# Kernel tuning notes

Measured on AMD Instinct MI355X. Metric: run time of the kernel, lower is better.

The kernel has to match this reference:

```python
import jax, jax.numpy as jnp
import numpy as np


def _apply_ring(x, angles):
    """Apply x @ R^T where R = G_0 @ G_1 @ ... @ G_{n-1} with ring planes
    (k, (k+1) % n). Equivalent to applying G_k^T to x for k = n-1 .. 0:
      x[:, k] <- c*x[:, k] - s*x[:, j]
      x[:, j] <- s*x[:, k] + c*x[:, j]
    x: [B, n], angles: [n].
    """
    n = angles.shape[0]

    def step(xT, k):
        a = angles[k]
        c, s = jnp.cos(a), jnp.sin(a)
        j = jnp.mod(k + 1, n)
        xi = xT[k]
        xj = xT[j]
        xT = xT.at[k].set(c * xi - s * xj)
        xT = xT.at[j].set(s * xi + c * xj)
        return xT, None

    ks = jnp.arange(n - 1, -1, -1)  # reverse order: R^T = G_{n-1}^T ... G_0^T
    xT, _ = jax.lax.scan(step, x.T, ks)  # carry is [n, B]
    return xT.T


def setup_inputs() -> dict:
    key = jax.random.key(0)
    k_x, k_e, k_d = jax.random.split(key, 3)
    B, n, num_blocks = 8192, 1024, 4
    return {
        "x": jax.random.normal(k_x, (B, n), dtype=jnp.float32),
        "angles_enc": jax.random.normal(k_e, (num_blocks, n), dtype=jnp.float32),
        "angles_dec": jax.random.normal(k_d, (num_blocks, n), dtype=jnp.float32),
        "hidden_weight": jnp.zeros((1,), dtype=jnp.float32),
        "hidden_state": jnp.zeros((n,), dtype=jnp.float32),
    }


def reference(x, angles_enc, angles_dec, hidden_weight, hidden_state):
    num_blocks = angles_enc.shape[0]
    b = x
    for blk in range(num_blocks):
        b = _apply_ring(b, angles_enc[blk])
    # recurrent blend; weight uses the detached hidden_weight (original uses
    # numpy on .detach()), so stop_gradient matches the original semantics.
    w = jax.nn.sigmoid(jax.lax.stop_gradient(hidden_weight[0]))
    bottleneck = (1.0 - w) * b + w * hidden_state[None, :]
    out = bottleneck
    for blk in range(num_blocks):
        out = _apply_ring(out, angles_dec[blk])
    return (bottleneck, out)
```

## Files before the change

### kernel.cpp

```cpp
#include <hip/hip_runtime.h>
#include <math.h>

#define N_COLS 1024
#define TPR    16
#define CHUNK  64
#define ROWS_PER_BLOCK 16
#define NRINGS 8

__global__ __launch_bounds__(256, 2)
void ClassicalEncoderDecoder_57080115363917_kernel(
        const float* __restrict__ x,
        const float* __restrict__ ae,
        const float* __restrict__ ad,
        const float* __restrict__ hw,
        const float* __restrict__ hs,
        float* __restrict__ out, int B)
{
    __shared__ float2 s_cs[NRINGS * CHUNK * TPR];
    __shared__ float  s_A [NRINGS * TPR];
    __shared__ float2 s_aux[NRINGS];

    const int tid = threadIdx.x;

    for (int i = 0; i < 32; ++i) {
        int idx = i * 256 + tid;
        int r   = idx >> 10;
        int k   = idx & 1023;
        const float* ang = (r < 4) ? (ae + (r << 10)) : (ad + ((r - 4) << 10));
        float a = ang[k];
        float sv, cv;
        sincosf(a, &sv, &cv);
        int t = k >> 6, j = k & 63;
        float2 e = make_float2(cv, sv);
        if (k == 1023) {
            s_aux[r] = e;
            e = make_float2(0.f, -1.f);
        }
        s_cs[(r * CHUNK + j) * TPR + t] = e;
    }
    __syncthreads();
    if (tid < NRINGS * TPR) {
        int r = tid >> 4, t = tid & 15;
        float p = 1.f;
        for (int j = 0; j < CHUNK; ++j) p *= -s_cs[(r * CHUNK + j) * TPR + t].y;
        s_A[tid] = p;
    }
    __syncthreads();

    const int lane      = tid & 63;
    const int g         = lane >> 4;
    const int t         = lane & 15;
    const int groupBase = lane & 48;
    const int row       = blockIdx.x * ROWS_PER_BLOCK + (tid >> 6) * 4 + g;

    const float* xr = x + (size_t)row * N_COLS + t * CHUNK;
    float y[CHUNK];
    #pragma unroll
    for (int i = 0; i < 16; ++i) {
        float4 v = ((const float4*)xr)[i];
        y[4*i+0] = v.x; y[4*i+1] = v.y; y[4*i+2] = v.z; y[4*i+3] = v.w;
    }

    const float w   = 1.f / (1.f + expf(-hw[0]));
    const float omw = 1.f - w;

    for (int r = 0; r < NRINGS; ++r) {
        if (r == 4) {
            float4* ob = (float4*)(out + (size_t)row * N_COLS + t * CHUNK);
            const float4* hp = (const float4*)(hs + t * CHUNK);
            #pragma unroll
            for (int i = 0; i < 16; ++i) {
                float4 h = hp[i];
                float4 bn;
                bn.x = fmaf(omw, y[4*i+0], w * h.x);
                bn.y = fmaf(omw, y[4*i+1], w * h.y);
                bn.z = fmaf(omw, y[4*i+2], w * h.z);
                bn.w = fmaf(omw, y[4*i+3], w * h.w);
                ob[i] = bn;
                y[4*i+0] = bn.x; y[4*i+1] = bn.y; y[4*i+2] = bn.z; y[4*i+3] = bn.w;
            }
        }

        const float2* csr = s_cs + r * CHUNK * TPR;
        const float2  cN  = s_aux[r];

        float y0 = __shfl(y[0],  groupBase);
        float yN = __shfl(y[63], groupBase + 15);
        float Cinit = cN.x * yN - cN.y * y0;
        float x0n   = fmaf(cN.y, yN, cN.x * y0);
        if (t == 0) y[0] = x0n;

        float carry = 0.f;
        float ztmp  = 0.f;
        #pragma unroll
        for (int j = CHUNK - 1; j >= 0; --j) {
            float2 cs = csr[j * TPR + t];
            float z   = fmaf(cs.y, y[j], cs.x * carry);
            carry     = fmaf(-cs.y, carry, cs.x * y[j]);
            if (j == CHUNK - 1) ztmp = z; else y[j + 1] = z;
        }

        float sa = s_A[r * TPR + t], sb = carry;
        #pragma unroll
        for (int d = 1; d < 16; d <<= 1) {
            float a2 = __shfl_down(sa, d);
            float b2 = __shfl_down(sb, d);
            if (t + d < 16) { sb = fmaf(sa, b2, sb); sa *= a2; }
        }
        float ea = __shfl_down(sa, 1);
        float eb = __shfl_down(sb, 1);
        float z0  = fmaf(sa, Cinit, sb);
        float Cin = (t == 15) ? Cinit : fmaf(ea, Cinit, eb);

        float P = 1.f;
        #pragma unroll
        for (int j = CHUNK - 1; j >= 0; --j) {
            float2 cs = csr[j * TPR + t];
            float f = cs.x * P;
            P = -cs.y * P;
            if (j == CHUNK - 1) ztmp = fmaf(f, Cin, ztmp);
            else                y[j + 1] = fmaf(f, Cin, y[j + 1]);
        }

        float up = __shfl_up(ztmp, 1);
        y[0] = (t == 0) ? z0 : up;
    }

    float4* oo = (float4*)(out + (size_t)B * N_COLS + (size_t)row * N_COLS + t * CHUNK);
    #pragma unroll
    for (int i = 0; i < 16; ++i) {
        float4 v;
        v.x = y[4*i+0]; v.y = y[4*i+1]; v.z = y[4*i+2]; v.w = y[4*i+3];
        oo[i] = v;
    }
}

extern "C" void kernel_launch(void* const* d_in, const int* in_sizes, int n_in,
                              void* d_out, int out_size, void* d_ws, size_t ws_size,
                              hipStream_t stream) {
    const float* x  = (const float*)d_in[0];
    const float* ae = (const float*)d_in[1];
    const float* ad = (const float*)d_in[2];
    const float* hw = (const float*)d_in[3];
    const float* hs = (const float*)d_in[4];
    float* out = (float*)d_out;

    const int B = in_sizes[0] / N_COLS;
    dim3 grid(B / ROWS_PER_BLOCK), block(256);
    hipLaunchKernelGGL(ClassicalEncoderDecoder_57080115363917_kernel,
                       grid, block, 0, stream, x, ae, ad, hw, hs, out, B);
}
```

Before: 133.3 us.

## Precompute Givens coefficients in a setup kernel and halve per-thread chunk size

Adds a small setup kernel that computes sin/cos, the propagation factors and the chunk products once into workspace, so the main kernel no longer repeats the sincos work and shared-memory staging in every block. The main kernel uses 32 threads per row with 32-element chunks, which cuts per-thread register pressure enough to raise launch bounds to 4 blocks per SM. Coefficients are read as float4 from global/L2 instead of LDS, and the scan now has 5 shuffle steps instead of 4. The old kernel is kept as a fallback when the workspace is too small.

```diff
diff --git a/kernel.cpp b/kernel.cpp
--- a/kernel.cpp
+++ b/kernel.cpp
@@ -2,47 +2,200 @@
 #include <math.h>
 
 #define N_COLS 1024
-#define TPR    16
-#define CHUNK  64
-#define ROWS_PER_BLOCK 16
 #define NRINGS 8
 
+#define TPR    32
+#define CHUNK  32
+#define ROWS_PER_BLOCK 8
+
+#define F_OFF   16384
+#define A_OFF   24576
+#define AUX_OFF 24832
+#define WS_FLOATS 24848
+
+__global__ void ced_setup(const float* __restrict__ ae,
+                          const float* __restrict__ ad,
+                          float* __restrict__ ws)
+{
+    __shared__ float2 ls[N_COLS];
+    const int r   = blockIdx.x;
+    const int tid = threadIdx.x;
+    const float* ang = (r < 4) ? (ae + (r << 10)) : (ad + ((r - 4) << 10));
+
+    #pragma unroll
+    for (int m = 0; m < 4; ++m) {
+        int k = tid * 4 + m;
+        float sv, cv;
+        sincosf(ang[k], &sv, &cv);
+        if (k == N_COLS - 1) {
+            ((float2*)(ws + AUX_OFF))[r] = make_float2(cv, sv);
+            cv = 0.f; sv = -1.f;
+        }
+        ls[k] = make_float2(cv, sv);
+    }
+    __syncthreads();
+
+    {
+        int k0 = tid * 4;
+        int t  = k0 >> 5;
+        int jp = (k0 & 31) >> 1;
+        float4* CS = (float4*)ws;
+        float2 e0 = ls[k0], e1 = ls[k0+1], e2 = ls[k0+2], e3 = ls[k0+3];
+        CS[(r*16 + jp    )*32 + t] = make_float4(e0.x, e0.y, e1.x, e1.y);
+        CS[(r*16 + jp + 1)*32 + t] = make_float4(e2.x, e2.y, e3.x, e3.y);
+    }
+
+    if (tid < TPR) {
+        int t = tid;
+        float f[CHUNK];
+        float P = 1.f;
+        for (int j = CHUNK - 1; j >= 0; --j) {
+            float2 cs = ls[t*CHUNK + j];
+            f[j] = cs.x * P;
+            P    = -cs.y * P;
+        }
+        float4* F = (float4*)(ws + F_OFF);
+        #pragma unroll
+        for (int qi = 0; qi < 8; ++qi)
+            F[(r*8 + qi)*32 + t] = make_float4(f[4*qi], f[4*qi+1], f[4*qi+2], f[4*qi+3]);
+        ws[A_OFF + r*TPR + t] = P;
+    }
+}
+
+__global__ __launch_bounds__(256, 4)
+void ced_main(const float* __restrict__ x,
+              const float* __restrict__ ws,
+              const float* __restrict__ hw,
+              const float* __restrict__ hs,
+              float* __restrict__ out, int B)
+{
+    const float4* CS  = (const float4*)ws;
+    const float4* F   = (const float4*)(ws + F_OFF);
+    const float*  A   = ws + A_OFF;
+    const float2* AUX = (const float2*)(ws + AUX_OFF);
+
+    const int tid  = threadIdx.x;
+    const int lane = tid & 63;
+    const int t    = lane & 31;
+    const int g    = lane >> 5;
+    const int groupBase = lane & 32;
+    const int row  = blockIdx.x * ROWS_PER_BLOCK + (tid >> 6) * 2 + g;
+
+    float y[CHUNK];
+    const float4* xp = (const float4*)(x + (size_t)row * N_COLS + t * CHUNK);
+    #pragma unroll
+    for (int i = 0; i < 8; ++i) {
+        float4 v = xp[i];
+        y[4*i] = v.x; y[4*i+1] = v.y; y[4*i+2] = v.z; y[4*i+3] = v.w;
+    }
+
+    const float w   = 1.f / (1.f + expf(-hw[0]));
+    const float omw = 1.f - w;
+
+    #pragma unroll 1
+    for (int r = 0; r < NRINGS; ++r) {
+        if (r == 4) {
+            float4* ob = (float4*)(out + (size_t)row * N_COLS + t * CHUNK);
+            const float4* hp = (const float4*)(hs + t * CHUNK);
+            #pragma unroll
+            for (int i = 0; i < 8; ++i) {
+                float4 h = hp[i];
+                float4 bn;
+                bn.x = fmaf(omw, y[4*i+0], w * h.x);
+                bn.y = fmaf(omw, y[4*i+1], w * h.y);
+                bn.z = fmaf(omw, y[4*i+2], w * h.z);
+                bn.w = fmaf(omw, y[4*i+3], w * h.w);
+                ob[i] = bn;
+                y[4*i+0] = bn.x; y[4*i+1] = bn.y; y[4*i+2] = bn.z; y[4*i+3] = bn.w;
+            }
+        }
+
+        const float2 cN = AUX[r];
+        float y0 = __shfl(y[0],       groupBase);
+        float yN = __shfl(y[CHUNK-1], groupBase + 31);
+        float Cinit = cN.x * yN - cN.y * y0;
+        float x0n   = fmaf(cN.y, yN, cN.x * y0);
+        if (t == 0) y[0] = x0n;
+
+        float carry = 0.f, ztmp = 0.f;
+        const float4* csr = CS + r * 512 + t;
+        #pragma unroll
+        for (int jp = CHUNK/2 - 1; jp >= 0; --jp) {
+            float4 cs4 = csr[jp * 32];
+            const int j1 = 2*jp + 1;
+            float z1 = fmaf(cs4.w, y[j1], cs4.z * carry);
+            carry    = fmaf(-cs4.w, carry, cs4.z * y[j1]);
+            if (j1 == CHUNK - 1) ztmp = z1; else y[j1+1] = z1;
+            const int j0 = 2*jp;
+            float z0s = fmaf(cs4.y, y[j0], cs4.x * carry);
+            carry     = fmaf(-cs4.y, carry, cs4.x * y[j0]);
+            y[j0+1] = z0s;
+        }
+
+        float sa = A[r*32 + t];
+        float sb = carry;
+        #pragma unroll
+        for (int d = 1; d < TPR; d <<= 1) {
+            float a2 = __shfl_down(sa, d);
+            float b2 = __shfl_down(sb, d);
+            if (t + d < TPR) { sb = fmaf(sa, b2, sb); sa *= a2; }
+        }
+        float ea = __shfl_down(sa, 1), eb = __shfl_down(sb, 1);
+        float zfirst = fmaf(sa, Cinit, sb);
+        float Cin = (t == TPR - 1) ? Cinit : fmaf(ea, Cinit, eb);
+
+        const float4* fr = F + r * 256 + t;
+        #pragma unroll
+        for (int qi = CHUNK/4 - 1; qi >= 0; --qi) {
+            float4 f4 = fr[qi * 32];
+            const int j = 4*qi;
+            if (j + 3 == CHUNK - 1) ztmp   = fmaf(f4.w, Cin, ztmp);
+            else                    y[j+4] = fmaf(f4.w, Cin, y[j+4]);
+            y[j+3] = fmaf(f4.z, Cin, y[j+3]);
+            y[j+2] = fmaf(f4.y, Cin, y[j+2]);
+            y[j+1] = fmaf(f4.x, Cin, y[j+1]);
+        }
+
+        float up = __shfl_up(ztmp, 1);
+        y[0] = (t == 0) ? zfirst : up;
+    }
+
+    float4* oo = (float4*)(out + (size_t)B * N_COLS + (size_t)row * N_COLS + t * CHUNK);
+    #pragma unroll
+    for (int i = 0; i < 8; ++i)
+        oo[i] = make_float4(y[4*i], y[4*i+1], y[4*i+2], y[4*i+3]);
+}
+
 __global__ __launch_bounds__(256, 2)
-void ClassicalEncoderDecoder_57080115363917_kernel(
-        const float* __restrict__ x,
-        const float* __restrict__ ae,
-        const float* __restrict__ ad,
-        const float* __restrict__ hw,
-        const float* __restrict__ hs,
-        float* __restrict__ out, int B)
+void ced_fallback(const float* __restrict__ x,
+                  const float* __restrict__ ae,
+                  const float* __restrict__ ad,
+                  const float* __restrict__ hw,
+                  const float* __restrict__ hs,
+                  float* __restrict__ out, int B)
 {
-    __shared__ float2 s_cs[NRINGS * CHUNK * TPR];
-    __shared__ float  s_A [NRINGS * TPR];
+    __shared__ float2 s_cs[NRINGS * 64 * 16];
+    __shared__ float  s_A [NRINGS * 16];
     __shared__ float2 s_aux[NRINGS];
 
     const int tid = threadIdx.x;
-
     for (int i = 0; i < 32; ++i) {
         int idx = i * 256 + tid;
         int r   = idx >> 10;
         int k   = idx & 1023;
         const float* ang = (r < 4) ? (ae + (r << 10)) : (ad + ((r - 4) << 10));
-        float a = ang[k];
         float sv, cv;
-        sincosf(a, &sv, &cv);
+        sincosf(ang[k], &sv, &cv);
         int t = k >> 6, j = k & 63;
         float2 e = make_float2(cv, sv);
-        if (k == 1023) {
-            s_aux[r] = e;
-            e = make_float2(0.f, -1.f);
-        }
-        s_cs[(r * CHUNK + j) * TPR + t] = e;
+        if (k == 1023) { s_aux[r] = e; e = make_float2(0.f, -1.f); }
+        s_cs[(r * 64 + j) * 16 + t] = e;
     }
     __syncthreads();
-    if (tid < NRINGS * TPR) {
+    if (tid < NRINGS * 16) {
         int r = tid >> 4, t = tid & 15;
         float p = 1.f;
-        for (int j = 0; j < CHUNK; ++j) p *= -s_cs[(r * CHUNK + j) * TPR + t].y;
+        for (int j = 0; j < 64; ++j) p *= -s_cs[(r * 64 + j) * 16 + t].y;
         s_A[tid] = p;
     }
     __syncthreads();
@@ -51,23 +204,22 @@
     const int g         = lane >> 4;
     const int t         = lane & 15;
     const int groupBase = lane & 48;
-    const int row       = blockIdx.x * ROWS_PER_BLOCK + (tid >> 6) * 4 + g;
-
-    const float* xr = x + (size_t)row * N_COLS + t * CHUNK;
-    float y[CHUNK];
+    const int row       = blockIdx.x * 16 + (tid >> 6) * 4 + g;
+
+    const float* xr = x + (size_t)row * N_COLS + t * 64;
+    float y[64];
     #pragma unroll
     for (int i = 0; i < 16; ++i) {
         float4 v = ((const float4*)xr)[i];
-        y[4*i+0] = v.x; y[4*i+1] = v.y; y[4*i+2] = v.z; y[4*i+3] = v.w;
-    }
-
+        y[4*i] = v.x; y[4*i+1] = v.y; y[4*i+2] = v.z; y[4*i+3] = v.w;
+    }
     const float w   = 1.f / (1.f + expf(-hw[0]));
     const float omw = 1.f - w;
 
     for (int r = 0; r < NRINGS; ++r) {
         if (r == 4) {
-            float4* ob = (float4*)(out + (size_t)row * N_COLS + t * CHUNK);
-            const float4* hp = (const float4*)(hs + t * CHUNK);
+            float4* ob = (float4*)(out + (size_t)row * N_COLS + t * 64);
+            const float4* hp = (const float4*)(hs + t * 64);
             #pragma unroll
             for (int i = 0; i < 16; ++i) {
                 float4 h = hp[i];
@@ -80,27 +232,23 @@
                 y[4*i+0] = bn.x; y[4*i+1] = bn.y; y[4*i+2] = bn.z; y[4*i+3] = bn.w;
             }
         }
-
-        const float2* csr = s_cs + r * CHUNK * TPR;
+        const float2* csr = s_cs + r * 64 * 16;
         const float2  cN  = s_aux[r];
-
         float y0 = __shfl(y[0],  groupBase);
         float yN = __shfl(y[63], groupBase + 15);
         float Cinit = cN.x * yN - cN.y * y0;
         float x0n   = fmaf(cN.y, yN, cN.x * y0);
         if (t == 0) y[0] = x0n;
 
-        float carry = 0.f;
-        float ztmp  = 0.f;
-        #pragma unroll
-        for (int j = CHUNK - 1; j >= 0; --j) {
-            float2 cs = csr[j * TPR + t];
+        float carry = 0.f, ztmp = 0.f;
+        #pragma unroll
+        for (int j = 63; j >= 0; --j) {
+            float2 cs = csr[j * 16 + t];
             float z   = fmaf(cs.y, y[j], cs.x * carry);
             carry     = fmaf(-cs.y, carry, cs.x * y[j]);
-            if (j == CHUNK - 1) ztmp = z; else y[j + 1] = z;
-        }
-
-        float sa = s_A[r * TPR + t], sb = carry;
+            if (j == 63) ztmp = z; else y[j + 1] = z;
+        }
+        float sa = s_A[r * 16 + t], sb = carry;
         #pragma unroll
         for (int d = 1; d < 16; d <<= 1) {
             float a2 = __shfl_down(sa, d);
@@ -114,25 +262,21 @@
 
         float P = 1.f;
         #pragma unroll
-        for (int j = CHUNK - 1; j >= 0; --j) {
-            float2 cs = csr[j * TPR + t];
+        for (int j = 63; j >= 0; --j) {
+            float2 cs = csr[j * 16 + t];
             float f = cs.x * P;
             P = -cs.y * P;
-            if (j == CHUNK - 1) ztmp = fmaf(f, Cin, ztmp);
-            else                y[j + 1] = fmaf(f, Cin, y[j + 1]);
-        }
-
+            if (j == 63) ztmp = fmaf(f, Cin, ztmp);
+            else         y[j + 1] = fmaf(f, Cin, y[j + 1]);
+        }
         float up = __shfl_up(ztmp, 1);
         y[0] = (t == 0) ? z0 : up;
     }
 
-    float4* oo = (float4*)(out + (size_t)B * N_COLS + (size_t)row * N_COLS + t * CHUNK);
-    #pragma unroll
-    for (int i = 0; i < 16; ++i) {
-        float4 v;
-        v.x = y[4*i+0]; v.y = y[4*i+1]; v.z = y[4*i+2]; v.w = y[4*i+3];
-        oo[i] = v;
-    }
+    float4* oo = (float4*)(out + (size_t)B * N_COLS + (size_t)row * N_COLS + t * 64);
+    #pragma unroll
+    for (int i = 0; i < 16; ++i)
+        oo[i] = make_float4(y[4*i], y[4*i+1], y[4*i+2], y[4*i+3]);
 }
 
 extern "C" void kernel_launch(void* const* d_in, const int* in_sizes, int n_in,
@@ -144,9 +288,15 @@
     const float* hw = (const float*)d_in[3];
     const float* hs = (const float*)d_in[4];
     float* out = (float*)d_out;
-
     const int B = in_sizes[0] / N_COLS;
-    dim3 grid(B / ROWS_PER_BLOCK), block(256);
-    hipLaunchKernelGGL(ClassicalEncoderDecoder_57080115363917_kernel,
-                       grid, block, 0, stream, x, ae, ad, hw, hs, out, B);
+
+    if (ws_size >= WS_FLOATS * sizeof(float)) {
+        hipLaunchKernelGGL(ced_setup, dim3(NRINGS), dim3(256), 0, stream,
+                           ae, ad, (float*)d_ws);
+        hipLaunchKernelGGL(ced_main, dim3(B / ROWS_PER_BLOCK), dim3(256), 0, stream,
+                           x, (const float*)d_ws, hw, hs, out, B);
+    } else {
+        hipLaunchKernelGGL(ced_fallback, dim3(B / 16), dim3(256), 0, stream,
+                           x, ae, ad, hw, hs, out, B);
+    }
 }
```

After: 137.3 us. +3.0%, slower.

## Process two rows per thread group with double-buffered per-ring coefficient tables

Applied to the files above, without the earlier changes.

Each 32-thread group now handles two rows at once, with 32 columns per thread instead of 64. This halves the serial chain length per ring and shares the cosine/sine and scan-coefficient loads across both rows. Coefficient tables are built one ring at a time into double-buffered shared memory, so the build overlaps the current ring's work instead of all eight being precomputed up front. The prefix factors are now precomputed once per ring rather than recomputed per row, which cuts shared memory and per-row multiplies. The cost is a __syncthreads per ring and some recomputation of sincos in every block.

```diff
diff --git a/kernel.cpp b/kernel.cpp
--- a/kernel.cpp
+++ b/kernel.cpp
@@ -2,136 +2,202 @@
 #include <math.h>
 
 #define N_COLS 1024
-#define TPR    16
-#define CHUNK  64
-#define ROWS_PER_BLOCK 16
 #define NRINGS 8
 
+#define TPR    32
+#define CHUNK  32
+#define PAIRS_PER_BLOCK 8
+
 __global__ __launch_bounds__(256, 2)
-void ClassicalEncoderDecoder_57080115363917_kernel(
-        const float* __restrict__ x,
-        const float* __restrict__ ae,
-        const float* __restrict__ ad,
-        const float* __restrict__ hw,
-        const float* __restrict__ hs,
-        float* __restrict__ out, int B)
+void ced_fused(const float* __restrict__ x,
+               const float* __restrict__ ae,
+               const float* __restrict__ ad,
+               const float* __restrict__ hw,
+               const float* __restrict__ hs,
+               float* __restrict__ out, int B)
 {
-    __shared__ float2 s_cs[NRINGS * CHUNK * TPR];
-    __shared__ float  s_A [NRINGS * TPR];
-    __shared__ float2 s_aux[NRINGS];
-
-    const int tid = threadIdx.x;
-
-    for (int i = 0; i < 32; ++i) {
-        int idx = i * 256 + tid;
-        int r   = idx >> 10;
-        int k   = idx & 1023;
-        const float* ang = (r < 4) ? (ae + (r << 10)) : (ad + ((r - 4) << 10));
-        float a = ang[k];
-        float sv, cv;
-        sincosf(a, &sv, &cv);
-        int t = k >> 6, j = k & 63;
-        float2 e = make_float2(cv, sv);
-        if (k == 1023) {
-            s_aux[r] = e;
-            e = make_float2(0.f, -1.f);
-        }
-        s_cs[(r * CHUNK + j) * TPR + t] = e;
-    }
-    __syncthreads();
-    if (tid < NRINGS * TPR) {
-        int r = tid >> 4, t = tid & 15;
-        float p = 1.f;
-        for (int j = 0; j < CHUNK; ++j) p *= -s_cs[(r * CHUNK + j) * TPR + t].y;
-        s_A[tid] = p;
-    }
-    __syncthreads();
-
-    const int lane      = tid & 63;
-    const int g         = lane >> 4;
-    const int t         = lane & 15;
-    const int groupBase = lane & 48;
-    const int row       = blockIdx.x * ROWS_PER_BLOCK + (tid >> 6) * 4 + g;
-
-    const float* xr = x + (size_t)row * N_COLS + t * CHUNK;
-    float y[CHUNK];
-    #pragma unroll
-    for (int i = 0; i < 16; ++i) {
-        float4 v = ((const float4*)xr)[i];
-        y[4*i+0] = v.x; y[4*i+1] = v.y; y[4*i+2] = v.z; y[4*i+3] = v.w;
+    __shared__ float4 sCS[2][512];
+    __shared__ float4 sF [2][256];
+    __shared__ float  sA [2][32];
+    __shared__ float2 sAux[2];
+
+    const int tid  = threadIdx.x;
+    const int lane = tid & 63;
+    const int t    = lane & 31;
+    const int groupBase = lane & 32;
+    const int pairRow = blockIdx.x * PAIRS_PER_BLOCK + (tid >> 5);
+    const size_t rowA = (size_t)(2 * pairRow) * N_COLS;
+    const size_t rowB = rowA + N_COLS;
+
+    const int bt = tid >> 3;
+    const int bq = tid & 7;
+
+    float ya[CHUNK], yb[CHUNK];
+    {
+        const float4* xa = (const float4*)(x + rowA + t * CHUNK);
+        const float4* xb = (const float4*)(x + rowB + t * CHUNK);
+        #pragma unroll
+        for (int i = 0; i < 8; ++i) {
+            float4 va = xa[i], vb = xb[i];
+            ya[4*i] = va.x; ya[4*i+1] = va.y; ya[4*i+2] = va.z; ya[4*i+3] = va.w;
+            yb[4*i] = vb.x; yb[4*i+1] = vb.y; yb[4*i+2] = vb.z; yb[4*i+3] = vb.w;
+        }
     }
 
     const float w   = 1.f / (1.f + expf(-hw[0]));
     const float omw = 1.f - w;
 
+    auto build = [&](float4 av, int nb) {
+        float c0, s0, c1, s1, c2, s2, c3, s3;
+        sincosf(av.x, &s0, &c0);
+        sincosf(av.y, &s1, &c1);
+        sincosf(av.z, &s2, &c2);
+        sincosf(av.w, &s3, &c3);
+        if (tid == 255) {
+            sAux[nb] = make_float2(c3, s3);
+            c3 = 0.f; s3 = -1.f;
+        }
+        sCS[nb][(2*bq    )*32 + bt] = make_float4(c0, s0, c1, s1);
+        sCS[nb][(2*bq + 1)*32 + bt] = make_float4(c2, s2, c3, s3);
+
+        float f3 = c3;       float P = -s3;
+        float f2 = c2 * P;   P *= -s2;
+        float f1 = c1 * P;   P *= -s1;
+        float f0 = c0 * P;   P *= -s0;
+
+        float ip = P;
+        #pragma unroll
+        for (int d = 1; d < 8; d <<= 1) {
+            float tmp = __shfl_down(ip, d);
+            if (bq + d < 8) ip *= tmp;
+        }
+        float ex = __shfl_down(ip, 1);
+        if (bq == 7) ex = 1.f;
+        sF[nb][bq*32 + bt] = make_float4(f0*ex, f1*ex, f2*ex, f3*ex);
+        if (bq == 0) sA[nb][bt] = ip;
+    };
+
+    build(*(const float4*)(ae + tid * 4), 0);
+    __syncthreads();
+
+    #pragma unroll 1
     for (int r = 0; r < NRINGS; ++r) {
+        const int buf = r & 1;
+
+        float4 av;
+        if (r < NRINGS - 1) {
+            const int rr = r + 1;
+            const float* base = (rr < 4) ? (ae + (rr << 10)) : (ad + ((rr - 4) << 10));
+            av = *(const float4*)(base + tid * 4);
+        }
+
         if (r == 4) {
-            float4* ob = (float4*)(out + (size_t)row * N_COLS + t * CHUNK);
+            float4* oa = (float4*)(out + rowA + t * CHUNK);
+            float4* ob = (float4*)(out + rowB + t * CHUNK);
             const float4* hp = (const float4*)(hs + t * CHUNK);
             #pragma unroll
-            for (int i = 0; i < 16; ++i) {
+            for (int i = 0; i < 8; ++i) {
                 float4 h = hp[i];
-                float4 bn;
-                bn.x = fmaf(omw, y[4*i+0], w * h.x);
-                bn.y = fmaf(omw, y[4*i+1], w * h.y);
-                bn.z = fmaf(omw, y[4*i+2], w * h.z);
-                bn.w = fmaf(omw, y[4*i+3], w * h.w);
-                ob[i] = bn;
-                y[4*i+0] = bn.x; y[4*i+1] = bn.y; y[4*i+2] = bn.z; y[4*i+3] = bn.w;
+                float4 na, nb2;
+                na.x  = fmaf(omw, ya[4*i+0], w * h.x);
+                na.y  = fmaf(omw, ya[4*i+1], w * h.y);
+                na.z  = fmaf(omw, ya[4*i+2], w * h.z);
+                na.w  = fmaf(omw, ya[4*i+3], w * h.w);
+                nb2.x = fmaf(omw, yb[4*i+0], w * h.x);
+                nb2.y = fmaf(omw, yb[4*i+1], w * h.y);
+                nb2.z = fmaf(omw, yb[4*i+2], w * h.z);
+                nb2.w = fmaf(omw, yb[4*i+3], w * h.w);
+                oa[i] = na; ob[i] = nb2;
+                ya[4*i+0] = na.x;  ya[4*i+1] = na.y;  ya[4*i+2] = na.z;  ya[4*i+3] = na.w;
+                yb[4*i+0] = nb2.x; yb[4*i+1] = nb2.y; yb[4*i+2] = nb2.z; yb[4*i+3] = nb2.w;
             }
         }
 
-        const float2* csr = s_cs + r * CHUNK * TPR;
-        const float2  cN  = s_aux[r];
-
-        float y0 = __shfl(y[0],  groupBase);
-        float yN = __shfl(y[63], groupBase + 15);
-        float Cinit = cN.x * yN - cN.y * y0;
-        float x0n   = fmaf(cN.y, yN, cN.x * y0);
-        if (t == 0) y[0] = x0n;
-
-        float carry = 0.f;
-        float ztmp  = 0.f;
-        #pragma unroll
-        for (int j = CHUNK - 1; j >= 0; --j) {
-            float2 cs = csr[j * TPR + t];
-            float z   = fmaf(cs.y, y[j], cs.x * carry);
-            carry     = fmaf(-cs.y, carry, cs.x * y[j]);
-            if (j == CHUNK - 1) ztmp = z; else y[j + 1] = z;
-        }
-
-        float sa = s_A[r * TPR + t], sb = carry;
-        #pragma unroll
-        for (int d = 1; d < 16; d <<= 1) {
-            float a2 = __shfl_down(sa, d);
-            float b2 = __shfl_down(sb, d);
-            if (t + d < 16) { sb = fmaf(sa, b2, sb); sa *= a2; }
-        }
-        float ea = __shfl_down(sa, 1);
-        float eb = __shfl_down(sb, 1);
-        float z0  = fmaf(sa, Cinit, sb);
-        float Cin = (t == 15) ? Cinit : fmaf(ea, Cinit, eb);
-
-        float P = 1.f;
-        #pragma unroll
-        for (int j = CHUNK - 1; j >= 0; --j) {
-            float2 cs = csr[j * TPR + t];
-            float f = cs.x * P;
-            P = -cs.y * P;
-            if (j == CHUNK - 1) ztmp = fmaf(f, Cin, ztmp);
-            else                y[j + 1] = fmaf(f, Cin, y[j + 1]);
-        }
-
-        float up = __shfl_up(ztmp, 1);
-        y[0] = (t == 0) ? z0 : up;
+        const float4* csL = sCS[buf];
+        const float4* fL  = sF [buf];
+        const float2  cN  = sAux[buf];
+        const float   saI = sA[buf][t];
+
+        float y0a = __shfl(ya[0],       groupBase);
+        float yNa = __shfl(ya[CHUNK-1], groupBase + 31);
+        float y0b = __shfl(yb[0],       groupBase);
+        float yNb = __shfl(yb[CHUNK-1], groupBase + 31);
+        float CinitA = cN.x * yNa - cN.y * y0a;
+        float CinitB = cN.x * yNb - cN.y * y0b;
+        float x0nA   = fmaf(cN.y, yNa, cN.x * y0a);
+        float x0nB   = fmaf(cN.y, yNb, cN.x * y0b);
+        if (t == 0) { ya[0] = x0nA; yb[0] = x0nB; }
+
+        float carA = 0.f, carB = 0.f, ztA = 0.f, ztB = 0.f;
+        #pragma unroll
+        for (int jp = CHUNK/2 - 1; jp >= 0; --jp) {
+            float4 cs4 = csL[jp * 32 + t];
+            const int j1 = 2*jp + 1;
+            float z1a = fmaf(cs4.w, ya[j1], cs4.z * carA);
+            float z1b = fmaf(cs4.w, yb[j1], cs4.z * carB);
+            carA = fmaf(-cs4.w, carA, cs4.z * ya[j1]);
+            carB = fmaf(-cs4.w, carB, cs4.z * yb[j1]);
+            if (j1 == CHUNK - 1) { ztA = z1a; ztB = z1b; }
+            else                 { ya[j1+1] = z1a; yb[j1+1] = z1b; }
+            const int j0 = 2*jp;
+            float z0a = fmaf(cs4.y, ya[j0], cs4.x * carA);
+            float z0b = fmaf(cs4.y, yb[j0], cs4.x * carB);
+            carA = fmaf(-cs4.y, carA, cs4.x * ya[j0]);
+            carB = fmaf(-cs4.y, carB, cs4.x * yb[j0]);
+            ya[j0+1] = z0a; yb[j0+1] = z0b;
+        }
+
+        float sa = saI;
+        float sbA = carA, sbB = carB;
+        #pragma unroll
+        for (int d = 1; d < TPR; d <<= 1) {
+            float a2  = __shfl_down(sa,  d);
+            float b2a = __shfl_down(sbA, d);
+            float b2b = __shfl_down(sbB, d);
+            if (t + d < TPR) {
+                sbA = fmaf(sa, b2a, sbA);
+                sbB = fmaf(sa, b2b, sbB);
+                sa *= a2;
+            }
+        }
+        float ea  = __shfl_down(sa,  1);
+        float ebA = __shfl_down(sbA, 1);
+        float ebB = __shfl_down(sbB, 1);
+        float zfA = fmaf(sa, CinitA, sbA);
+        float zfB = fmaf(sa, CinitB, sbB);
+        float CinA = (t == TPR - 1) ? CinitA : fmaf(ea, CinitA, ebA);
+        float CinB = (t == TPR - 1) ? CinitB : fmaf(ea, CinitB, ebB);
+
+        #pragma unroll
+        for (int qi = CHUNK/4 - 1; qi >= 0; --qi) {
+            float4 f4 = fL[qi * 32 + t];
+            const int j = 4*qi;
+            if (j + 3 == CHUNK - 1) { ztA = fmaf(f4.w, CinA, ztA);
+                                      ztB = fmaf(f4.w, CinB, ztB); }
+            else                    { ya[j+4] = fmaf(f4.w, CinA, ya[j+4]);
+                                      yb[j+4] = fmaf(f4.w, CinB, yb[j+4]); }
+            ya[j+3] = fmaf(f4.z, CinA, ya[j+3]);  yb[j+3] = fmaf(f4.z, CinB, yb[j+3]);
+            ya[j+2] = fmaf(f4.y, CinA, ya[j+2]);  yb[j+2] = fmaf(f4.y, CinB, yb[j+2]);
+            ya[j+1] = fmaf(f4.x, CinA, ya[j+1]);  yb[j+1] = fmaf(f4.x, CinB, yb[j+1]);
+        }
+
+        float upA = __shfl_up(ztA, 1);
+        float upB = __shfl_up(ztB, 1);
+        ya[0] = (t == 0) ? zfA : upA;
+        yb[0] = (t == 0) ? zfB : upB;
+
+        if (r < NRINGS - 1) {
+            build(av, buf ^ 1);
+            __syncthreads();
+        }
     }
 
-    float4* oo = (float4*)(out + (size_t)B * N_COLS + (size_t)row * N_COLS + t * CHUNK);
+    float4* oa = (float4*)(out + (size_t)B * N_COLS + rowA + t * CHUNK);
+    float4* ob = (float4*)(out + (size_t)B * N_COLS + rowB + t * CHUNK);
     #pragma unroll
-    for (int i = 0; i < 16; ++i) {
-        float4 v;
-        v.x = y[4*i+0]; v.y = y[4*i+1]; v.z = y[4*i+2]; v.w = y[4*i+3];
-        oo[i] = v;
+    for (int i = 0; i < 8; ++i) {
+        oa[i] = make_float4(ya[4*i], ya[4*i+1], ya[4*i+2], ya[4*i+3]);
+        ob[i] = make_float4(yb[4*i], yb[4*i+1], yb[4*i+2], yb[4*i+3]);
     }
 }
 
@@ -144,9 +210,8 @@
     const float* hw = (const float*)d_in[3];
     const float* hs = (const float*)d_in[4];
     float* out = (float*)d_out;
-
     const int B = in_sizes[0] / N_COLS;
-    dim3 grid(B / ROWS_PER_BLOCK), block(256);
-    hipLaunchKernelGGL(ClassicalEncoderDecoder_57080115363917_kernel,
-                       grid, block, 0, stream, x, ae, ad, hw, hs, out, B);
+
+    hipLaunchKernelGGL(ced_fused, dim3(B / (2 * PAIRS_PER_BLOCK)), dim3(256),
+                       0, stream, x, ae, ad, hw, hs, out, B);
 }
```

After: 143.0 us. 1.07x slower.
